# Optimization experiments

Measured on AMD Instinct MI355X. Metric: run time of the kernel, lower is better.

Reference implementation:

```python
import jax, jax.numpy as jnp
import numpy as np

N = 100000
E = 3200000
IN_DIM = 256
HID = 128
OUT_DIM = 64


def setup_inputs() -> dict:
    key = jax.random.key(0)
    ks = jax.random.split(key, 8)
    features = jax.random.normal(ks[0], (N, IN_DIM), dtype=jnp.float32)
    edge_row = jax.random.randint(ks[1], (E,), 0, N, dtype=jnp.int32)
    edge_col = jax.random.randint(ks[2], (E,), 0, N, dtype=jnp.int32)
    edge_val = jax.random.uniform(ks[3], (E,), dtype=jnp.float32)
    W1 = jax.random.normal(ks[4], (IN_DIM, HID), dtype=jnp.float32) * (1.0 / np.sqrt(IN_DIM))
    b1 = jnp.zeros((HID,), dtype=jnp.float32)
    W2 = jax.random.normal(ks[5], (HID, OUT_DIM), dtype=jnp.float32) * (1.0 / np.sqrt(HID))
    b2 = jnp.zeros((OUT_DIM,), dtype=jnp.float32)
    return {"features": features, "edge_row": edge_row, "edge_col": edge_col,
            "edge_val": edge_val, "W1": W1, "b1": b1, "W2": W2, "b2": b2}


def reference(features, edge_row, edge_col, edge_val, W1, b1, W2, b2):
    # fc1: [N, IN_DIM] @ [IN_DIM, HID] + b1
    h = features @ W1 + b1                                   # [N, HID]
    # spmm(A, h): for each edge (r, c, v): out[r] += v * h[c]
    msgs = edge_val[:, None] * h[edge_col]                    # [E, HID] gather
    h = jax.ops.segment_sum(msgs, edge_row, num_segments=N)   # [N, HID] scatter-add
    h = jax.nn.relu(h)
    h = h @ W2 + b2                                           # [N, OUT_DIM]
    return jax.nn.log_softmax(h, axis=1)
```

## Files before the change

kernel.cpp:

```cpp
#include <hip/hip_runtime.h>
#include <math.h>

constexpr int IN_DIM  = 256;
constexpr int HID     = 128;
constexpr int OUT_DIM = 64;

constexpr int BROWS   = 128;
constexpr int NBUCK   = 782;
constexpr int CAP     = 4608;
constexpr int CAP2    = 5504;
constexpr int CHUNK   = 8192;
constexpr int GC_STRIDE = 16;

typedef short  bf16x8 __attribute__((ext_vector_type(8)));
typedef float  f32x4  __attribute__((ext_vector_type(4)));
typedef float  f32x2  __attribute__((ext_vector_type(2)));
typedef int    i32x4  __attribute__((ext_vector_type(4)));

__device__ __forceinline__ unsigned short f2bf(float x) {
    union { float f; unsigned u; } v; v.f = x;
    unsigned r = v.u + 0x7FFF + ((v.u >> 16) & 1);
    return (unsigned short)(r >> 16);
}

__global__ __launch_bounds__(256) void wt_kernel(const float* __restrict__ W1,
                                                 const float* __restrict__ W2,
                                                 unsigned short* __restrict__ W1T,
                                                 unsigned short* __restrict__ W2T)
{
    int idx = blockIdx.x * 256 + threadIdx.x;
    if (idx < IN_DIM * HID) {
        int k = idx >> 7;
        int n = idx & 127;
        W1T[n * IN_DIM + k] = f2bf(W1[idx]);
    } else {
        int j = idx - IN_DIM * HID;
        int k = j >> 6;
        int n = j & 63;
        W2T[n * HID + k] = f2bf(W2[j]);
    }
}

__global__ __launch_bounds__(256) void fc1_mfma(const float* __restrict__ feat,
                                                const unsigned short* __restrict__ W1T,
                                                const float* __restrict__ b1,
                                                unsigned short* __restrict__ h1b, int N)
{
    const int t    = threadIdx.x;
    const int lane = t & 63;
    const int w    = t >> 6;
    const int quad = lane >> 4;
    const int ln15 = lane & 15;
    const int row0 = blockIdx.x * 64;

    int arow = row0 + w * 16 + ln15;
    if (arow >= N) arow = N - 1;
    const float* aptr = feat + (size_t)arow * IN_DIM + quad * 8;

    f32x4 acc[8];
#pragma unroll
    for (int i = 0; i < 8; ++i) acc[i] = (f32x4){0.f, 0.f, 0.f, 0.f};

#pragma unroll
    for (int ks = 0; ks < 8; ++ks) {
        float4 a0 = *(const float4*)(aptr + ks * 32);
        float4 a1 = *(const float4*)(aptr + ks * 32 + 4);
        bf16x8 afrag;
        afrag[0] = (short)f2bf(a0.x); afrag[1] = (short)f2bf(a0.y);
        afrag[2] = (short)f2bf(a0.z); afrag[3] = (short)f2bf(a0.w);
        afrag[4] = (short)f2bf(a1.x); afrag[5] = (short)f2bf(a1.y);
        afrag[6] = (short)f2bf(a1.z); afrag[7] = (short)f2bf(a1.w);
#pragma unroll
        for (int nt = 0; nt < 8; ++nt) {
            bf16x8 bfrag = *(const bf16x8*)&W1T[(size_t)(nt * 16 + ln15) * IN_DIM + ks * 32 + quad * 8];
            acc[nt] = __builtin_amdgcn_mfma_f32_16x16x32_bf16(afrag, bfrag, acc[nt], 0, 0, 0);
        }
    }

#pragma unroll
    for (int nt = 0; nt < 8; ++nt) {
        int col = nt * 16 + ln15;
        float bias = b1[col];
#pragma unroll
        for (int r = 0; r < 4; ++r) {
            int grow = row0 + w * 16 + quad * 4 + r;
            if (grow < N)
                h1b[(size_t)grow * HID + col] = f2bf(acc[nt][r] + bias);
        }
    }
}

__global__ __launch_bounds__(1024) void bin_kernel(const int* __restrict__ erow,
                                                   const int* __restrict__ ecol,
                                                   const float* __restrict__ eval,
                                                   int* __restrict__ gCursor,
                                                   int2* __restrict__ binned, int E)
{
    __shared__ int sCnt[NBUCK];
    __shared__ int sBase[NBUCK];
    const int t = threadIdx.x;
    const int e0 = blockIdx.x * CHUNK;
    const int eEnd = min(e0 + CHUNK, E);

    for (int i = t; i < NBUCK; i += 1024) sCnt[i] = 0;
    __syncthreads();

    for (int e = e0 + t; e < eEnd; e += 1024)
        atomicAdd(&sCnt[erow[e] >> 7], 1);
    __syncthreads();

    for (int i = t; i < NBUCK; i += 1024) {
        int c = sCnt[i];
        sBase[i] = c ? atomicAdd(&gCursor[i * GC_STRIDE], c) : 0;
        sCnt[i] = 0;
    }
    __syncthreads();

    for (int e = e0 + t; e < eEnd; e += 1024) {
        int   r = erow[e];
        int   c = ecol[e];
        float v = eval[e];
        int   b = r >> 7;
        int off = sBase[b] + atomicAdd(&sCnt[b], 1);
        if (off < CAP)
            binned[(size_t)b * CAP + off] = make_int2((c << 8) | ((r & 127) << 25),
                                                      __float_as_int(v));
    }
}

__global__ __launch_bounds__(256) void sort_bucket4(const int* __restrict__ gCursor,
                                                    const int2* __restrict__ binned,
                                                    int2* __restrict__ edges2,
                                                    int2* __restrict__ rowIdx, int N)
{
    __shared__ int2 sE[CAP];
    __shared__ int sHist[BROWS];
    __shared__ int sStart[BROWS + 1];
    __shared__ int sCur[BROWS];
    const int t  = threadIdx.x;
    const int b  = blockIdx.x;
    const int nE = min(gCursor[b * GC_STRIDE], CAP);
    const size_t baseIn  = (size_t)b * CAP;
    const size_t baseOut = (size_t)b * CAP2;

    if (t < BROWS) sHist[t] = 0;
    __syncthreads();

    for (int i = t; i < nE; i += 256) {
        int2 p = binned[baseIn + i];
        sE[i] = p;
        atomicAdd(&sHist[(unsigned)p.x >> 25], 1);
    }
    __syncthreads();

    if (t < BROWS) sStart[t + 1] = (sHist[t] + 7) & ~7;
    if (t == 0) sStart[0] = 0;
    __syncthreads();
    for (int o = 1; o < BROWS; o <<= 1) {
        int v = 0;
        if (t < BROWS) {
            v = sStart[t + 1];
            if (t >= o) v += sStart[t + 1 - o];
        }
        __syncthreads();
        if (t < BROWS) sStart[t + 1] = v;
        __syncthreads();
    }
    if (t < BROWS) sCur[t] = sStart[t];
    __syncthreads();

    for (int i = t; i < nE; i += 256) {
        int2 p = sE[i];
        int rl = (unsigned)p.x >> 25;
        int pos = atomicAdd(&sCur[rl], 1);
        edges2[baseOut + pos] = p;
    }

    if (t < BROWS) {
        int h  = sHist[t];
        int ph = (h + 7) & ~7;
        size_t p0 = baseOut + sStart[t];
        for (int k = h; k < ph; ++k)
            edges2[p0 + k] = make_int2(0, 0);
        int rr = b * BROWS + t;
        if (rr < N)
            rowIdx[rr] = make_int2((int)p0, (int)(p0 + ph));
    }
}

__global__ __launch_bounds__(256) void spmm_kernel(const int2* __restrict__ rowIdx,
                                                   const int2* __restrict__ edges2,
                                                   const unsigned short* __restrict__ h1b,
                                                   unsigned* __restrict__ h2b, int N)
{
    const int lane  = threadIdx.x & 63;
    const int lane4 = lane * 4;
    const int r     = (blockIdx.x * blockDim.x + threadIdx.x) >> 6;
    if (r >= N) return;
    const char* h1base = (const char*)h1b;

    const int2 se = rowIdx[r];
    int j = se.x;
    const int jend = se.y;
    f32x2 acc = (f32x2){0.f, 0.f};

    for (; j + 16 <= jend; j += 16) {
        i32x4 q[8];
#pragma unroll
        for (int u = 0; u < 8; ++u)
            q[u] = __builtin_nontemporal_load((const i32x4*)&edges2[j + u * 2]);
        unsigned g[16];
#pragma unroll
        for (int u = 0; u < 8; ++u) {
            g[2 * u]     = *(const unsigned*)(h1base + (q[u].x & 0x01FFFFFF) + lane4);
            g[2 * u + 1] = *(const unsigned*)(h1base + (q[u].z & 0x01FFFFFF) + lane4);
        }
#pragma unroll
        for (int u = 0; u < 8; ++u) {
            f32x2 h0 = (f32x2){__uint_as_float(g[2 * u] << 16),
                               __uint_as_float(g[2 * u] & 0xFFFF0000u)};
            f32x2 h1 = (f32x2){__uint_as_float(g[2 * u + 1] << 16),
                               __uint_as_float(g[2 * u + 1] & 0xFFFF0000u)};
            acc += h0 * __int_as_float(q[u].y);
            acc += h1 * __int_as_float(q[u].w);
        }
    }
    if (j < jend) {
        i32x4 q[4];
#pragma unroll
        for (int u = 0; u < 4; ++u)
            q[u] = __builtin_nontemporal_load((const i32x4*)&edges2[j + u * 2]);
        unsigned g[8];
#pragma unroll
        for (int u = 0; u < 4; ++u) {
            g[2 * u]     = *(const unsigned*)(h1base + (q[u].x & 0x01FFFFFF) + lane4);
            g[2 * u + 1] = *(const unsigned*)(h1base + (q[u].z & 0x01FFFFFF) + lane4);
        }
#pragma unroll
        for (int u = 0; u < 4; ++u) {
            f32x2 h0 = (f32x2){__uint_as_float(g[2 * u] << 16),
                               __uint_as_float(g[2 * u] & 0xFFFF0000u)};
            f32x2 h1 = (f32x2){__uint_as_float(g[2 * u + 1] << 16),
                               __uint_as_float(g[2 * u + 1] & 0xFFFF0000u)};
            acc += h0 * __int_as_float(q[u].y);
            acc += h1 * __int_as_float(q[u].w);
        }
    }

    float ax = fmaxf(acc.x, 0.f), ay = fmaxf(acc.y, 0.f);
    h2b[(size_t)r * 64 + lane] = (unsigned)f2bf(ax) | ((unsigned)f2bf(ay) << 16);
}

__global__ __launch_bounds__(256) void fc2_mfma(const unsigned short* __restrict__ h2b,
                                                const unsigned short* __restrict__ W2T,
                                                const float* __restrict__ b2,
                                                float* __restrict__ out, int N)
{
    const int t    = threadIdx.x;
    const int lane = t & 63;
    const int w    = t >> 6;
    const int quad = lane >> 4;
    const int ln15 = lane & 15;
    const int row0 = blockIdx.x * 64;

    int arow = row0 + w * 16 + ln15;
    if (arow >= N) arow = N - 1;

    f32x4 acc[4];
#pragma unroll
    for (int i = 0; i < 4; ++i) acc[i] = (f32x4){0.f, 0.f, 0.f, 0.f};

#pragma unroll
    for (int ks = 0; ks < 4; ++ks) {
        bf16x8 afrag = *(const bf16x8*)&h2b[(size_t)arow * HID + ks * 32 + quad * 8];
#pragma unroll
        for (int nt = 0; nt < 4; ++nt) {
            bf16x8 bfrag = *(const bf16x8*)&W2T[(size_t)(nt * 16 + ln15) * HID + ks * 32 + quad * 8];
            acc[nt] = __builtin_amdgcn_mfma_f32_16x16x32_bf16(afrag, bfrag, acc[nt], 0, 0, 0);
        }
    }

    float bias[4];
#pragma unroll
    for (int nt = 0; nt < 4; ++nt) bias[nt] = b2[nt * 16 + ln15];

#pragma unroll
    for (int r = 0; r < 4; ++r) {
        float v[4];
#pragma unroll
        for (int nt = 0; nt < 4; ++nt) v[nt] = acc[nt][r] + bias[nt];

        float m = fmaxf(fmaxf(v[0], v[1]), fmaxf(v[2], v[3]));
#pragma unroll
        for (int o = 1; o < 16; o <<= 1) m = fmaxf(m, __shfl_xor(m, o));
        float s = __expf(v[0] - m) + __expf(v[1] - m) +
                  __expf(v[2] - m) + __expf(v[3] - m);
#pragma unroll
        for (int o = 1; o < 16; o <<= 1) s += __shfl_xor(s, o);
        float ls = __logf(s);

        int grow = row0 + w * 16 + quad * 4 + r;
        if (grow < N) {
#pragma unroll
            for (int nt = 0; nt < 4; ++nt)
                out[(size_t)grow * OUT_DIM + nt * 16 + ln15] = v[nt] - m - ls;
        }
    }
}

extern "C" void kernel_launch(void* const* d_in, const int* in_sizes, int n_in,
                              void* d_out, int out_size, void* d_ws, size_t ws_size,
                              hipStream_t stream) {
    const float* feat = (const float*)d_in[0];
    const int*   erow = (const int*)d_in[1];
    const int*   ecol = (const int*)d_in[2];
    const float* eval = (const float*)d_in[3];
    const float* W1   = (const float*)d_in[4];
    const float* b1   = (const float*)d_in[5];
    const float* W2   = (const float*)d_in[6];
    const float* b2   = (const float*)d_in[7];
    float*       out  = (float*)d_out;

    const int N = in_sizes[0] / IN_DIM;
    const int E = in_sizes[1];

    unsigned short* h1b    = (unsigned short*)d_ws;
    unsigned short* h2b    = h1b + (size_t)N * HID;
    int2*           binned = (int2*)(h2b + (size_t)N * HID);
    int2*           edges2 = binned + (size_t)NBUCK * CAP;
    int2*           rowIdx = edges2 + (size_t)NBUCK * CAP2;
    unsigned short* W1T    = (unsigned short*)(rowIdx + N);
    unsigned short* W2T    = W1T + IN_DIM * HID;
    int*            gCursor= (int*)(W2T + HID * OUT_DIM);

    hipMemsetAsync(gCursor, 0, NBUCK * GC_STRIDE * sizeof(int), stream);

    wt_kernel<<<(IN_DIM * HID + HID * OUT_DIM) / 256, 256, 0, stream>>>(W1, W2, W1T, W2T);
    fc1_mfma<<<(N + 63) / 64, 256, 0, stream>>>(feat, W1T, b1, h1b, N);
    bin_kernel<<<(E + CHUNK - 1) / CHUNK, 1024, 0, stream>>>(erow, ecol, eval,
                                                             gCursor, binned, E);
    sort_bucket4<<<NBUCK, 256, 0, stream>>>(gCursor, binned, edges2, rowIdx, N);

    const int nblk = (N + 3) / 4;
    spmm_kernel<<<nblk, 256, 0, stream>>>(rowIdx, edges2, h1b,
                                          (unsigned*)h2b, N);
    fc2_mfma<<<(N + 63) / 64, 256, 0, stream>>>(h2b, W2T, b2, out, N);
}
```

Before: 469.4 us.

## Tile two row blocks per wave in fc1 and pad bin slots to 8-edge runs

fc1 now computes 128 rows per block: each wave handles two 16-row tiles and reuses the same W1T fragments for both, which halves redundant weight loads and the block count. The bin kernel reserves per-block bucket space rounded up to multiples of 8 and fills the unused slots with -1 sentinels, which sort_bucket4 skips. This makes each block's writes into a bucket start on 8-entry aligned boundaries, but it raises CAP, the binned workspace and shared-memory use in sort_bucket4, and adds padding writes. Holding two accumulator sets also doubles register pressure in fc1.

```diff
diff --git a/kernel.cpp b/kernel.cpp
--- a/kernel.cpp
+++ b/kernel.cpp
@@ -7,7 +7,7 @@
 
 constexpr int BROWS   = 128;
 constexpr int NBUCK   = 782;
-constexpr int CAP     = 4608;
+constexpr int CAP     = 5984;
 constexpr int CAP2    = 5504;
 constexpr int CHUNK   = 8192;
 constexpr int GC_STRIDE = 16;
@@ -51,41 +51,63 @@
     const int w    = t >> 6;
     const int quad = lane >> 4;
     const int ln15 = lane & 15;
-    const int row0 = blockIdx.x * 64;
-
-    int arow = row0 + w * 16 + ln15;
-    if (arow >= N) arow = N - 1;
-    const float* aptr = feat + (size_t)arow * IN_DIM + quad * 8;
-
-    f32x4 acc[8];
-#pragma unroll
-    for (int i = 0; i < 8; ++i) acc[i] = (f32x4){0.f, 0.f, 0.f, 0.f};
+    const int row0 = blockIdx.x * 128;
+
+    int ar0 = row0 + w * 16 + ln15;
+    int ar1 = ar0 + 64;
+    if (ar0 >= N) ar0 = N - 1;
+    if (ar1 >= N) ar1 = N - 1;
+    const float* ap0 = feat + (size_t)ar0 * IN_DIM + quad * 8;
+    const float* ap1 = feat + (size_t)ar1 * IN_DIM + quad * 8;
+
+    f32x4 acc[2][8];
+#pragma unroll
+    for (int rt = 0; rt < 2; ++rt)
+#pragma unroll
+        for (int i = 0; i < 8; ++i) acc[rt][i] = (f32x4){0.f, 0.f, 0.f, 0.f};
 
 #pragma unroll
     for (int ks = 0; ks < 8; ++ks) {
-        float4 a0 = *(const float4*)(aptr + ks * 32);
-        float4 a1 = *(const float4*)(aptr + ks * 32 + 4);
-        bf16x8 afrag;
-        afrag[0] = (short)f2bf(a0.x); afrag[1] = (short)f2bf(a0.y);
-        afrag[2] = (short)f2bf(a0.z); afrag[3] = (short)f2bf(a0.w);
-        afrag[4] = (short)f2bf(a1.x); afrag[5] = (short)f2bf(a1.y);
-        afrag[6] = (short)f2bf(a1.z); afrag[7] = (short)f2bf(a1.w);
+        bf16x8 bf[8];
+#pragma unroll
+        for (int nt = 0; nt < 8; ++nt)
+            bf[nt] = *(const bf16x8*)&W1T[(size_t)(nt * 16 + ln15) * IN_DIM + ks * 32 + quad * 8];
+
+        float4 a0 = *(const float4*)(ap0 + ks * 32);
+        float4 a1 = *(const float4*)(ap0 + ks * 32 + 4);
+        bf16x8 af0;
+        af0[0] = (short)f2bf(a0.x); af0[1] = (short)f2bf(a0.y);
+        af0[2] = (short)f2bf(a0.z); af0[3] = (short)f2bf(a0.w);
+        af0[4] = (short)f2bf(a1.x); af0[5] = (short)f2bf(a1.y);
+        af0[6] = (short)f2bf(a1.z); af0[7] = (short)f2bf(a1.w);
+
+        float4 a2 = *(const float4*)(ap1 + ks * 32);
+        float4 a3 = *(const float4*)(ap1 + ks * 32 + 4);
+        bf16x8 af1;
+        af1[0] = (short)f2bf(a2.x); af1[1] = (short)f2bf(a2.y);
+        af1[2] = (short)f2bf(a2.z); af1[3] = (short)f2bf(a2.w);
+        af1[4] = (short)f2bf(a3.x); af1[5] = (short)f2bf(a3.y);
+        af1[6] = (short)f2bf(a3.z); af1[7] = (short)f2bf(a3.w);
+
 #pragma unroll
         for (int nt = 0; nt < 8; ++nt) {
-            bf16x8 bfrag = *(const bf16x8*)&W1T[(size_t)(nt * 16 + ln15) * IN_DIM + ks * 32 + quad * 8];
-            acc[nt] = __builtin_amdgcn_mfma_f32_16x16x32_bf16(afrag, bfrag, acc[nt], 0, 0, 0);
-        }
-    }
-
-#pragma unroll
-    for (int nt = 0; nt < 8; ++nt) {
-        int col = nt * 16 + ln15;
-        float bias = b1[col];
-#pragma unroll
-        for (int r = 0; r < 4; ++r) {
-            int grow = row0 + w * 16 + quad * 4 + r;
-            if (grow < N)
-                h1b[(size_t)grow * HID + col] = f2bf(acc[nt][r] + bias);
+            acc[0][nt] = __builtin_amdgcn_mfma_f32_16x16x32_bf16(af0, bf[nt], acc[0][nt], 0, 0, 0);
+            acc[1][nt] = __builtin_amdgcn_mfma_f32_16x16x32_bf16(af1, bf[nt], acc[1][nt], 0, 0, 0);
+        }
+    }
+
+#pragma unroll
+    for (int rt = 0; rt < 2; ++rt) {
+#pragma unroll
+        for (int nt = 0; nt < 8; ++nt) {
+            int col = nt * 16 + ln15;
+            float bias = b1[col];
+#pragma unroll
+            for (int r = 0; r < 4; ++r) {
+                int grow = row0 + rt * 64 + w * 16 + quad * 4 + r;
+                if (grow < N)
+                    h1b[(size_t)grow * HID + col] = f2bf(acc[rt][nt][r] + bias);
+            }
         }
     }
 }
@@ -110,8 +132,9 @@
     __syncthreads();
 
     for (int i = t; i < NBUCK; i += 1024) {
-        int c = sCnt[i];
-        sBase[i] = c ? atomicAdd(&gCursor[i * GC_STRIDE], c) : 0;
+        int c  = sCnt[i];
+        int cp = (c + 7) & ~7;
+        sBase[i] = c ? atomicAdd(&gCursor[i * GC_STRIDE], cp) : 0;
         sCnt[i] = 0;
     }
     __syncthreads();
@@ -126,6 +149,18 @@
             binned[(size_t)b * CAP + off] = make_int2((c << 8) | ((r & 127) << 25),
                                                       __float_as_int(v));
     }
+    __syncthreads();
+
+    for (int i = t; i < NBUCK; i += 1024) {
+        int c = sCnt[i];
+        if (c & 7) {
+            int base = sBase[i];
+            int cp   = (c + 7) & ~7;
+            for (int k = c; k < cp; ++k)
+                if (base + k < CAP)
+                    binned[(size_t)i * CAP + base + k] = make_int2(-1, 0);
+        }
+    }
 }
 
 __global__ __launch_bounds__(256) void sort_bucket4(const int* __restrict__ gCursor,
@@ -149,7 +184,8 @@
     for (int i = t; i < nE; i += 256) {
         int2 p = binned[baseIn + i];
         sE[i] = p;
-        atomicAdd(&sHist[(unsigned)p.x >> 25], 1);
+        if (p.x != -1)
+            atomicAdd(&sHist[(unsigned)p.x >> 25], 1);
     }
     __syncthreads();
 
@@ -171,6 +207,7 @@
 
     for (int i = t; i < nE; i += 256) {
         int2 p = sE[i];
+        if (p.x == -1) continue;
         int rl = (unsigned)p.x >> 25;
         int pos = atomicAdd(&sCur[rl], 1);
         edges2[baseOut + pos] = p;
@@ -336,7 +373,7 @@
     hipMemsetAsync(gCursor, 0, NBUCK * GC_STRIDE * sizeof(int), stream);
 
     wt_kernel<<<(IN_DIM * HID + HID * OUT_DIM) / 256, 256, 0, stream>>>(W1, W2, W1T, W2T);
-    fc1_mfma<<<(N + 63) / 64, 256, 0, stream>>>(feat, W1T, b1, h1b, N);
+    fc1_mfma<<<(N + 127) / 128, 256, 0, stream>>>(feat, W1T, b1, h1b, N);
     bin_kernel<<<(E + CHUNK - 1) / CHUNK, 1024, 0, stream>>>(erow, ecol, eval,
                                                              gCursor, binned, E);
     sort_bucket4<<<NBUCK, 256, 0, stream>>>(gCursor, binned, edges2, rowIdx, N);
```

New measurement: 472.0 us. Within noise of the previous version (+0.5%).

## Fuse fc1 GEMM and edge binning into one interleaved launch

Applied to the files above, without the earlier changes.

Merges the fc1 MFMA kernel and the edge bucketing kernel into a single launch whose blocks alternate between the two roles, so the compute-bound GEMM and the memory- and atomic-bound binning can overlap on the GPU. The bin block size drops from 1024 to 256 threads and the chunk from 8192 to 2048 edges to match. Smaller chunks mean more global atomics on the bucket cursors and more scattered partial writes per bucket, and the shared-memory arrays are now allocated for fc1 blocks too.

```diff
diff --git a/kernel.cpp b/kernel.cpp
--- a/kernel.cpp
+++ b/kernel.cpp
@@ -9,7 +9,7 @@
 constexpr int NBUCK   = 782;
 constexpr int CAP     = 4608;
 constexpr int CAP2    = 5504;
-constexpr int CHUNK   = 8192;
+constexpr int CHUNK2  = 2048;
 constexpr int GC_STRIDE = 16;
 
 typedef short  bf16x8 __attribute__((ext_vector_type(8)));
@@ -41,90 +41,102 @@
     }
 }
 
-__global__ __launch_bounds__(256) void fc1_mfma(const float* __restrict__ feat,
-                                                const unsigned short* __restrict__ W1T,
-                                                const float* __restrict__ b1,
-                                                unsigned short* __restrict__ h1b, int N)
-{
-    const int t    = threadIdx.x;
-    const int lane = t & 63;
-    const int w    = t >> 6;
-    const int quad = lane >> 4;
-    const int ln15 = lane & 15;
-    const int row0 = blockIdx.x * 64;
-
-    int arow = row0 + w * 16 + ln15;
-    if (arow >= N) arow = N - 1;
-    const float* aptr = feat + (size_t)arow * IN_DIM + quad * 8;
-
-    f32x4 acc[8];
-#pragma unroll
-    for (int i = 0; i < 8; ++i) acc[i] = (f32x4){0.f, 0.f, 0.f, 0.f};
-
-#pragma unroll
-    for (int ks = 0; ks < 8; ++ks) {
-        float4 a0 = *(const float4*)(aptr + ks * 32);
-        float4 a1 = *(const float4*)(aptr + ks * 32 + 4);
-        bf16x8 afrag;
-        afrag[0] = (short)f2bf(a0.x); afrag[1] = (short)f2bf(a0.y);
-        afrag[2] = (short)f2bf(a0.z); afrag[3] = (short)f2bf(a0.w);
-        afrag[4] = (short)f2bf(a1.x); afrag[5] = (short)f2bf(a1.y);
-        afrag[6] = (short)f2bf(a1.z); afrag[7] = (short)f2bf(a1.w);
-#pragma unroll
-        for (int nt = 0; nt < 8; ++nt) {
-            bf16x8 bfrag = *(const bf16x8*)&W1T[(size_t)(nt * 16 + ln15) * IN_DIM + ks * 32 + quad * 8];
-            acc[nt] = __builtin_amdgcn_mfma_f32_16x16x32_bf16(afrag, bfrag, acc[nt], 0, 0, 0);
-        }
-    }
-
-#pragma unroll
-    for (int nt = 0; nt < 8; ++nt) {
-        int col = nt * 16 + ln15;
-        float bias = b1[col];
-#pragma unroll
-        for (int r = 0; r < 4; ++r) {
-            int grow = row0 + w * 16 + quad * 4 + r;
-            if (grow < N)
-                h1b[(size_t)grow * HID + col] = f2bf(acc[nt][r] + bias);
-        }
-    }
-}
-
-__global__ __launch_bounds__(1024) void bin_kernel(const int* __restrict__ erow,
-                                                   const int* __restrict__ ecol,
-                                                   const float* __restrict__ eval,
-                                                   int* __restrict__ gCursor,
-                                                   int2* __restrict__ binned, int E)
+__global__ __launch_bounds__(256) void fc1_bin_fused(
+        const float* __restrict__ feat,
+        const unsigned short* __restrict__ W1T,
+        const float* __restrict__ b1,
+        unsigned short* __restrict__ h1b, int N,
+        const int* __restrict__ erow,
+        const int* __restrict__ ecol,
+        const float* __restrict__ eval,
+        int* __restrict__ gCursor,
+        int2* __restrict__ binned, int E)
 {
     __shared__ int sCnt[NBUCK];
     __shared__ int sBase[NBUCK];
+
+    const int nfc1 = (N + 63) >> 6;
+    const int nbin = (E + CHUNK2 - 1) / CHUNK2;
+    const int nInter = 2 * min(nfc1, nbin);
+    const int b = blockIdx.x;
+
+    bool isBin;
+    int  id;
+    if (b < nInter) { isBin = (b & 1); id = b >> 1; }
+    else            { isBin = (nbin > nfc1); id = min(nfc1, nbin) + (b - nInter); }
+
     const int t = threadIdx.x;
-    const int e0 = blockIdx.x * CHUNK;
-    const int eEnd = min(e0 + CHUNK, E);
-
-    for (int i = t; i < NBUCK; i += 1024) sCnt[i] = 0;
-    __syncthreads();
-
-    for (int e = e0 + t; e < eEnd; e += 1024)
-        atomicAdd(&sCnt[erow[e] >> 7], 1);
-    __syncthreads();
-
-    for (int i = t; i < NBUCK; i += 1024) {
-        int c = sCnt[i];
-        sBase[i] = c ? atomicAdd(&gCursor[i * GC_STRIDE], c) : 0;
-        sCnt[i] = 0;
-    }
-    __syncthreads();
-
-    for (int e = e0 + t; e < eEnd; e += 1024) {
-        int   r = erow[e];
-        int   c = ecol[e];
-        float v = eval[e];
-        int   b = r >> 7;
-        int off = sBase[b] + atomicAdd(&sCnt[b], 1);
-        if (off < CAP)
-            binned[(size_t)b * CAP + off] = make_int2((c << 8) | ((r & 127) << 25),
-                                                      __float_as_int(v));
+
+    if (!isBin) {
+        const int lane = t & 63;
+        const int w    = t >> 6;
+        const int quad = lane >> 4;
+        const int ln15 = lane & 15;
+        const int row0 = id * 64;
+
+        int arow = row0 + w * 16 + ln15;
+        if (arow >= N) arow = N - 1;
+        const float* aptr = feat + (size_t)arow * IN_DIM + quad * 8;
+
+        f32x4 acc[8];
+#pragma unroll
+        for (int i = 0; i < 8; ++i) acc[i] = (f32x4){0.f, 0.f, 0.f, 0.f};
+
+#pragma unroll
+        for (int ks = 0; ks < 8; ++ks) {
+            float4 a0 = *(const float4*)(aptr + ks * 32);
+            float4 a1 = *(const float4*)(aptr + ks * 32 + 4);
+            bf16x8 afrag;
+            afrag[0] = (short)f2bf(a0.x); afrag[1] = (short)f2bf(a0.y);
+            afrag[2] = (short)f2bf(a0.z); afrag[3] = (short)f2bf(a0.w);
+            afrag[4] = (short)f2bf(a1.x); afrag[5] = (short)f2bf(a1.y);
+            afrag[6] = (short)f2bf(a1.z); afrag[7] = (short)f2bf(a1.w);
+#pragma unroll
+            for (int nt = 0; nt < 8; ++nt) {
+                bf16x8 bfrag = *(const bf16x8*)&W1T[(size_t)(nt * 16 + ln15) * IN_DIM + ks * 32 + quad * 8];
+                acc[nt] = __builtin_amdgcn_mfma_f32_16x16x32_bf16(afrag, bfrag, acc[nt], 0, 0, 0);
+            }
+        }
+
+#pragma unroll
+        for (int nt = 0; nt < 8; ++nt) {
+            int col = nt * 16 + ln15;
+            float bias = b1[col];
+#pragma unroll
+            for (int r = 0; r < 4; ++r) {
+                int grow = row0 + w * 16 + quad * 4 + r;
+                if (grow < N)
+                    h1b[(size_t)grow * HID + col] = f2bf(acc[nt][r] + bias);
+            }
+        }
+    } else {
+        const int e0   = id * CHUNK2;
+        const int eEnd = min(e0 + CHUNK2, E);
+
+        for (int i = t; i < NBUCK; i += 256) sCnt[i] = 0;
+        __syncthreads();
+
+        for (int e = e0 + t; e < eEnd; e += 256)
+            atomicAdd(&sCnt[erow[e] >> 7], 1);
+        __syncthreads();
+
+        for (int i = t; i < NBUCK; i += 256) {
+            int c = sCnt[i];
+            sBase[i] = c ? atomicAdd(&gCursor[i * GC_STRIDE], c) : 0;
+            sCnt[i] = 0;
+        }
+        __syncthreads();
+
+        for (int e = e0 + t; e < eEnd; e += 256) {
+            int   r = erow[e];
+            int   c = ecol[e];
+            float v = eval[e];
+            int   bk = r >> 7;
+            int off = sBase[bk] + atomicAdd(&sCnt[bk], 1);
+            if (off < CAP)
+                binned[(size_t)bk * CAP + off] = make_int2((c << 8) | ((r & 127) << 25),
+                                                           __float_as_int(v));
+        }
     }
 }
 
@@ -336,9 +348,13 @@
     hipMemsetAsync(gCursor, 0, NBUCK * GC_STRIDE * sizeof(int), stream);
 
     wt_kernel<<<(IN_DIM * HID + HID * OUT_DIM) / 256, 256, 0, stream>>>(W1, W2, W1T, W2T);
-    fc1_mfma<<<(N + 63) / 64, 256, 0, stream>>>(feat, W1T, b1, h1b, N);
-    bin_kernel<<<(E + CHUNK - 1) / CHUNK, 1024, 0, stream>>>(erow, ecol, eval,
-                                                             gCursor, binned, E);
+
+    const int nfc1 = (N + 63) / 64;
+    const int nbin = (E + CHUNK2 - 1) / CHUNK2;
+    fc1_bin_fused<<<nfc1 + nbin, 256, 0, stream>>>(feat, W1T, b1, h1b, N,
+                                                   erow, ecol, eval,
+                                                   gCursor, binned, E);
+
     sort_bucket4<<<NBUCK, 256, 0, stream>>>(gCursor, binned, edges2, rowIdx, N);
 
     const int nblk = (N + 3) / 4;
```

Result: no change. 477.7 us (+1.8%).
